# Optimization experiments

Measured on AMD Instinct MI355X. Metric: run time of the kernel, lower is better.

The kernel has to match this reference:

```python
import jax, jax.numpy as jnp
import numpy as np

B, SX, SL, D, H = 4, 4096, 256, 1024, 16
DH = D // H
LN_EPS = 1e-5
RMS_EPS = 1e-8


def layernorm(x, g, b):
    mu = jnp.mean(x, axis=-1, keepdims=True)
    var = jnp.mean(jnp.square(x - mu), axis=-1, keepdims=True)
    return (x - mu) * jax.lax.rsqrt(var + LN_EPS) * g + b


def rmsnorm(x, gamma):
    # torch: norm = ||x||_2 * dim^-0.5 ; x / clamp(norm, eps) * gamma
    norm = jnp.sqrt(jnp.sum(jnp.square(x), axis=-1, keepdims=True)) * (DH ** -0.5)
    return x / jnp.maximum(norm, RMS_EPS) * gamma


def setup_inputs() -> dict:
    key = jax.random.key(0)
    ks = jax.random.split(key, 6)
    s = 0.02
    return {
        "x": jax.random.normal(ks[0], (B, SX, D), jnp.float32),
        "latents": jax.random.normal(ks[1], (B, SL, D), jnp.float32),
        "mask_x": jnp.ones((B, SX), jnp.float32),
        "mask_latent": jnp.ones((B, SL), jnp.float32),
        "ln_x_g": jnp.ones((D,), jnp.float32),
        "ln_x_b": jnp.zeros((D,), jnp.float32),
        "ln_l_g": jnp.ones((D,), jnp.float32),
        "ln_l_b": jnp.zeros((D,), jnp.float32),
        "Wq": jax.random.normal(ks[2], (D, D), jnp.float32) * s,
        "Wkv": jax.random.normal(ks[3], (D, 2 * D), jnp.float32) * s,
        "qk_gamma": jnp.ones((DH,), jnp.float32),
        "Wo": jax.random.normal(ks[4], (D, D), jnp.float32) * s,
    }


def reference(x, latents, mask_x, mask_latent, ln_x_g, ln_x_b, ln_l_g, ln_l_b, Wq, Wkv, qk_gamma, Wo):
    xn = layernorm(x, ln_x_g, ln_x_b)                       # [B,SX,D]
    ln = layernorm(latents, ln_l_g, ln_l_b)                 # [B,SL,D]

    q = (ln @ Wq).reshape(B, SL, H, DH).transpose(0, 2, 1, 3)      # [B,H,SL,DH]
    kv_in = jnp.concatenate([xn, ln], axis=1)                      # [B,SX+SL,D]
    kv = kv_in @ Wkv
    Skv = SX + SL
    k = kv[..., :D].reshape(B, Skv, H, DH).transpose(0, 2, 1, 3)   # [B,H,Skv,DH]
    v = kv[..., D:].reshape(B, Skv, H, DH).transpose(0, 2, 1, 3)

    # NOTE: original code applies query_norm to BOTH q and k (faithful to source)
    q = rmsnorm(q, qk_gamma)
    k = rmsnorm(k, qk_gamma)

    scores = jnp.einsum("bhqd,bhkd->bhqk", q, k) / np.sqrt(DH)     # [B,H,SL,Skv]

    kv_mask = jnp.concatenate([mask_x, mask_latent], axis=1)       # [B,Skv]
    mask = kv_mask[:, None, :] * mask_latent[:, :, None]           # [B,SL,Skv]
    add_mask = (1.0 - mask)[:, None, :, :] * jnp.finfo(scores.dtype).min
    attn = jax.nn.softmax(scores + add_mask, axis=-1)

    y = jnp.einsum("bhqk,bhkd->bhqd", attn, v)                     # [B,H,SL,DH]
    y = y.transpose(0, 2, 1, 3).reshape(B, SL, D)
    return y @ Wo
```

## Files before the change

### kernel.cpp

```cpp
#include <hip/hip_runtime.h>

#define NB   4
#define SXX  4096
#define SLL  256
#define DD   1024
#define HH   16
#define DHH  64
#define SKV  4352
#define MKV  17408
#define NSPLIT 8

typedef __attribute__((ext_vector_type(8))) short bfrag;
typedef __attribute__((ext_vector_type(4))) float facc;

__device__ __forceinline__ unsigned short f2bf(float f){
  unsigned u = __builtin_bit_cast(unsigned, f);
  u = (u + 0x7fffu + ((u >> 16) & 1u)) >> 16;
  return (unsigned short)u;
}
__device__ __forceinline__ float bf2f(unsigned short h){
  unsigned u = ((unsigned)h) << 16;
  return __builtin_bit_cast(float, u);
}

#define GLOAD_LDS16(g, lds) __builtin_amdgcn_global_load_lds( \
    (const __attribute__((address_space(1))) unsigned int*)(const void*)(g), \
    (__attribute__((address_space(3))) unsigned int*)(void*)(lds), 16, 0, 0)

__global__ void wtrans3(const float* __restrict__ Wq, const float* __restrict__ Wkv,
                        const float* __restrict__ Wo, unsigned short* __restrict__ wqt,
                        unsigned short* __restrict__ wkvt, unsigned short* __restrict__ wot){
  __shared__ float t[32][33];
  int z = blockIdx.z;
  const float* in; unsigned short* out; int N;
  if (z == 0){ in = Wq;  out = wqt;  N = DD;   }
  else if (z == 1){ in = Wkv; out = wkvt; N = 2*DD; }
  else { in = Wo;  out = wot;  N = DD;   }
  int n0 = blockIdx.x * 32, k0 = blockIdx.y * 32;
  if (n0 >= N) return;
  int tx = threadIdx.x, ty = threadIdx.y;
  #pragma unroll
  for (int i = 0; i < 4; i++)
    t[ty + 8*i][tx] = in[(size_t)(k0 + ty + 8*i) * N + n0 + tx];
  __syncthreads();
  #pragma unroll
  for (int i = 0; i < 4; i++)
    out[(size_t)(n0 + ty + 8*i) * DD + k0 + tx] = f2bf(t[tx][ty + 8*i]);
}

__global__ void lnorm(const float* __restrict__ src, const float* __restrict__ g,
                      const float* __restrict__ bt, unsigned short* __restrict__ kvin,
                      unsigned short* __restrict__ dst2, int seq, int off){
  int row = blockIdx.x;
  int b = row / seq, s = row - b*seq;
  int t = threadIdx.x;
  const float4* rp = (const float4*)(src + (size_t)row * DD);
  float4 v = rp[t];
  float sum = v.x + v.y + v.z + v.w;
  float sq  = v.x*v.x + v.y*v.y + v.z*v.z + v.w*v.w;
  #pragma unroll
  for (int o = 32; o > 0; o >>= 1){ sum += __shfl_down(sum, o); sq += __shfl_down(sq, o); }
  __shared__ float ls[8];
  int w = t >> 6, l = t & 63;
  if (l == 0){ ls[w] = sum; ls[4 + w] = sq; }
  __syncthreads();
  sum = ls[0] + ls[1] + ls[2] + ls[3];
  sq  = ls[4] + ls[5] + ls[6] + ls[7];
  float mu  = sum * (1.f/DD);
  float var = sq * (1.f/DD) - mu*mu;
  float rs  = rsqrtf(var + 1e-5f);
  float4 gv = ((const float4*)g)[t];
  float4 bv = ((const float4*)bt)[t];
  ushort4 o4;
  o4.x = f2bf((v.x - mu)*rs*gv.x + bv.x);
  o4.y = f2bf((v.y - mu)*rs*gv.y + bv.y);
  o4.z = f2bf((v.z - mu)*rs*gv.z + bv.z);
  o4.w = f2bf((v.w - mu)*rs*gv.w + bv.w);
  *(ushort4*)(kvin + (size_t)(b*SKV + off + s) * DD + t*4) = o4;
  if (dst2) *(ushort4*)(dst2 + (size_t)row * DD + t*4) = o4;
}

__global__ __launch_bounds__(256) void gemm64(const unsigned short* __restrict__ A,
    const unsigned short* __restrict__ Bt, int M, int N, int K, float* __restrict__ outF){
  __shared__ unsigned short lA[64][72];
  __shared__ unsigned short lB[64][72];
  int n0 = blockIdx.x * 64, m0 = blockIdx.y * 64;
  int t = threadIdx.x, w = t >> 6, l = t & 63;
  int wr = (w >> 1) * 32, wc = (w & 1) * 32;
  int lr = l & 15, kq = (l >> 4) * 8;
  facc acc00 = (facc)0.f, acc01 = (facc)0.f, acc10 = (facc)0.f, acc11 = (facc)0.f;
  for (int k0 = 0; k0 < K; k0 += 64){
    #pragma unroll
    for (int cc = 0; cc < 2; cc++){
      int ch = t + cc*256;
      int row = ch >> 3, cg = (ch & 7) * 8;
      *(bfrag*)&lA[row][cg] = *(const bfrag*)&A[(size_t)(m0 + row) * K + k0 + cg];
      *(bfrag*)&lB[row][cg] = *(const bfrag*)&Bt[(size_t)(n0 + row) * K + k0 + cg];
    }
    __syncthreads();
    #pragma unroll
    for (int ks = 0; ks < 2; ks++){
      bfrag a0 = *(const bfrag*)&lA[wr + lr][ks*32 + kq];
      bfrag a1 = *(const bfrag*)&lA[wr + 16 + lr][ks*32 + kq];
      bfrag b0 = *(const bfrag*)&lB[wc + lr][ks*32 + kq];
      bfrag b1 = *(const bfrag*)&lB[wc + 16 + lr][ks*32 + kq];
      acc00 = __builtin_amdgcn_mfma_f32_16x16x32_bf16(a0, b0, acc00, 0, 0, 0);
      acc01 = __builtin_amdgcn_mfma_f32_16x16x32_bf16(a0, b1, acc01, 0, 0, 0);
      acc10 = __builtin_amdgcn_mfma_f32_16x16x32_bf16(a1, b0, acc10, 0, 0, 0);
      acc11 = __builtin_amdgcn_mfma_f32_16x16x32_bf16(a1, b1, acc11, 0, 0, 0);
    }
    __syncthreads();
  }
  int rl = (l >> 4) * 4, cl = l & 15;
  facc accs[2][2] = {{acc00, acc01},{acc10, acc11}};
  #pragma unroll
  for (int mt = 0; mt < 2; mt++)
  #pragma unroll
  for (int nt = 0; nt < 2; nt++)
  #pragma unroll
  for (int j = 0; j < 4; j++){
    int r = m0 + wr + mt*16 + rl + j;
    int c = n0 + wc + nt*16 + cl;
    outF[(size_t)r * N + c] = accs[mt][nt][j];
  }
}

__global__ __launch_bounds__(256) void gemm_q(const unsigned short* __restrict__ A,
    const unsigned short* __restrict__ Bt, const float* __restrict__ gamma,
    unsigned short* __restrict__ qn){
  __shared__ char smemb[18432];
  unsigned short* lA = (unsigned short*)smemb;
  unsigned short* lB = lA + 64*72;
  float* Cf = (float*)smemb;
  int h = blockIdx.x, n0 = h * 64, m0 = blockIdx.y * 64;
  int t = threadIdx.x, w = t >> 6, l = t & 63;
  int wr = (w >> 1) * 32, wc = (w & 1) * 32;
  int lr = l & 15, kq = (l >> 4) * 8;
  facc acc00 = (facc)0.f, acc01 = (facc)0.f, acc10 = (facc)0.f, acc11 = (facc)0.f;
  for (int k0 = 0; k0 < 1024; k0 += 64){
    #pragma unroll
    for (int cc = 0; cc < 2; cc++){
      int ch = t + cc*256;
      int row = ch >> 3, cg = (ch & 7) * 8;
      *(bfrag*)&lA[row*72 + cg] = *(const bfrag*)&A[(size_t)(m0 + row) * 1024 + k0 + cg];
      *(bfrag*)&lB[row*72 + cg] = *(const bfrag*)&Bt[(size_t)(n0 + row) * 1024 + k0 + cg];
    }
    __syncthreads();
    #pragma unroll
    for (int ks = 0; ks < 2; ks++){
      bfrag a0 = *(const bfrag*)&lA[(wr + lr)*72 + ks*32 + kq];
      bfrag a1 = *(const bfrag*)&lA[(wr + 16 + lr)*72 + ks*32 + kq];
      bfrag b0 = *(const bfrag*)&lB[(wc + lr)*72 + ks*32 + kq];
      bfrag b1 = *(const bfrag*)&lB[(wc + 16 + lr)*72 + ks*32 + kq];
      acc00 = __builtin_amdgcn_mfma_f32_16x16x32_bf16(a0, b0, acc00, 0, 0, 0);
      acc01 = __builtin_amdgcn_mfma_f32_16x16x32_bf16(a0, b1, acc01, 0, 0, 0);
      acc10 = __builtin_amdgcn_mfma_f32_16x16x32_bf16(a1, b0, acc10, 0, 0, 0);
      acc11 = __builtin_amdgcn_mfma_f32_16x16x32_bf16(a1, b1, acc11, 0, 0, 0);
    }
    __syncthreads();
  }
  int rl = (l >> 4) * 4, cl = l & 15;
  facc accs[2][2] = {{acc00, acc01},{acc10, acc11}};
  #pragma unroll
  for (int mt = 0; mt < 2; mt++)
  #pragma unroll
  for (int nt = 0; nt < 2; nt++)
  #pragma unroll
  for (int j = 0; j < 4; j++)
    Cf[(wr + mt*16 + rl + j)*66 + wc + nt*16 + cl] = accs[mt][nt][j];
  __syncthreads();
  if (t < 64){
    const float* src = &Cf[t*66];
    float ss = 0.f;
    #pragma unroll
    for (int d = 0; d < 64; d++){ float a = src[d]; ss = fmaf(a, a, ss); }
    float rv = 0.125f / fmaxf(sqrtf(ss) * 0.125f, 1e-8f);
    int r = m0 + t, b = r >> 8, sl = r & 255;
    unsigned short* dst = &qn[((size_t)(b*HH + h)*SLL + sl)*DHH];
    #pragma unroll
    for (int i = 0; i < 8; i++){
      ushort4 p; float g;
      g = gamma[i*8+0]; p.x = f2bf(src[i*8+0]*g*g*rv);
      g = gamma[i*8+1]; p.y = f2bf(src[i*8+1]*g*g*rv);
      g = gamma[i*8+2]; p.z = f2bf(src[i*8+2]*g*g*rv);
      g = gamma[i*8+3]; p.w = f2bf(src[i*8+3]*g*g*rv);
      ushort4 q;
      g = gamma[i*8+4]; q.x = f2bf(src[i*8+4]*g*g*rv);
      g = gamma[i*8+5]; q.y = f2bf(src[i*8+5]*g*g*rv);
      g = gamma[i*8+6]; q.z = f2bf(src[i*8+6]*g*g*rv);
      g = gamma[i*8+7]; q.w = f2bf(src[i*8+7]*g*g*rv);
      *(ushort4*)&dst[i*8]     = p;
      *(ushort4*)&dst[i*8 + 4] = q;
    }
  }
}

__global__ __launch_bounds__(256) void gemm_kv(const unsigned short* __restrict__ A,
    const unsigned short* __restrict__ Bt,
    const float* __restrict__ mask_x, const float* __restrict__ mask_lat,
    unsigned short* __restrict__ outK, unsigned short* __restrict__ outV,
    float* __restrict__ rkm){
  __shared__ unsigned short smem[128*136];
  unsigned short* lA = smem;
  unsigned short* lB = smem + 128*64;
  int n0 = blockIdx.x * 128, m0 = blockIdx.y * 128;
  int t = threadIdx.x, w = t >> 6, l = t & 63;
  int wr = (w >> 1) * 64, wc = (w & 1) * 64;
  int lr = l & 15, q2 = l >> 4;
  int r8 = l >> 3, u = l & 7;
  facc acc[4][4];
  #pragma unroll
  for (int mt = 0; mt < 4; mt++)
  #pragma unroll
  for (int nt = 0; nt < 4; nt++) acc[mt][nt] = (facc)0.f;
  const unsigned short* Ab = A  + (size_t)(m0 + w*32 + r8) * 1024 + (u ^ (r8 & 7)) * 8;
  const unsigned short* Bb = Bt + (size_t)(n0 + w*32 + r8) * 1024 + (u ^ (r8 & 7)) * 8;
  for (int k0 = 0; k0 < 1024; k0 += 64){
    #pragma unroll
    for (int i = 0; i < 4; i++){
      GLOAD_LDS16(Ab + (size_t)i*8*1024 + k0, &lA[(w*32 + i*8)*64]);
      GLOAD_LDS16(Bb + (size_t)i*8*1024 + k0, &lB[(w*32 + i*8)*64]);
    }
    __syncthreads();
    #pragma unroll
    for (int ks = 0; ks < 2; ks++){
      int su = ((ks*4 + q2) ^ (lr & 7)) * 8;
      bfrag av[4], bv[4];
      #pragma unroll
      for (int mt = 0; mt < 4; mt++) av[mt] = *(const bfrag*)&lA[(wr + mt*16 + lr)*64 + su];
      #pragma unroll
      for (int nt = 0; nt < 4; nt++) bv[nt] = *(const bfrag*)&lB[(wc + nt*16 + lr)*64 + su];
      #pragma unroll
      for (int mt = 0; mt < 4; mt++)
      #pragma unroll
      for (int nt = 0; nt < 4; nt++)
        acc[mt][nt] = __builtin_amdgcn_mfma_f32_16x16x32_bf16(av[mt], bv[nt], acc[mt][nt], 0, 0, 0);
    }
    __syncthreads();
  }
  int b = m0 / SKV, s0 = m0 - b*SKV;
  int rl = q2 * 4;
  if (blockIdx.x < 8){
    #pragma unroll
    for (int mt = 0; mt < 4; mt++)
    #pragma unroll
    for (int nt = 0; nt < 4; nt++)
    #pragma unroll
    for (int j = 0; j < 4; j++)
      smem[(wr + mt*16 + rl + j)*136 + wc + nt*16 + lr] = f2bf(acc[mt][nt][j]);
    __syncthreads();
    int s = t >> 1, hf = t & 1;
    int srow = s0 + s;
    float cm = (srow < SXX) ? mask_x[b*SXX + srow] : mask_lat[b*SLL + srow - SXX];
    const unsigned short* src = &smem[s*136 + hf*64];
    uint4 wv[8];
    #pragma unroll
    for (int i = 0; i < 8; i++) wv[i] = *(const uint4*)&src[i*8];
    float ss0 = 0.f, ss1 = 0.f;
    #pragma unroll
    for (int i = 0; i < 8; i++){
      const unsigned short* pp = (const unsigned short*)&wv[i];
      #pragma unroll
      for (int e = 0; e < 4; e++){
        float a = bf2f(pp[e]);     ss0 = fmaf(a, a, ss0);
        float c = bf2f(pp[e + 4]); ss1 = fmaf(c, c, ss1);
      }
    }
    float rv = 1.f / fmaxf(sqrtf(ss0 + ss1) * 0.125f, 1e-8f);
    int h = (n0 >> 6) + hf;
    unsigned short* dst = &outK[((size_t)(b*HH + h)*SKV + srow)*DHH];
    #pragma unroll
    for (int i = 0; i < 8; i++)
      *(uint4*)&dst[i*8] = wv[i];
    rkm[((size_t)(b*HH + h))*SKV + srow] = (cm != 0.f) ? rv : -1.f;
  } else {
    #pragma unroll
    for (int mt = 0; mt < 4; mt++)
    #pragma unroll
    for (int nt = 0; nt < 4; nt++){
      ushort4 p;
      p.x = f2bf(acc[mt][nt][0]); p.y = f2bf(acc[mt][nt][1]);
      p.z = f2bf(acc[mt][nt][2]); p.w = f2bf(acc[mt][nt][3]);
      *(ushort4*)&smem[(wc + nt*16 + lr)*136 + wr + mt*16 + rl] = p;
    }
    __syncthreads();
    int c = t >> 1, hf = t & 1;
    int hh = ((n0 - DD) >> 6) + (c >> 6), d = c & 63;
    const unsigned short* src = &smem[c*136 + hf*64];
    unsigned short* dst = &outV[((size_t)(b*HH + hh)*DHH + d)*SKV + s0 + hf*64];
    #pragma unroll
    for (int i = 0; i < 8; i++)
      *(uint4*)&dst[i*8] = *(const uint4*)&src[i*8];
  }
}

__global__ __launch_bounds__(256) void attn(const unsigned short* __restrict__ qn,
    const unsigned short* __restrict__ kbuf, const unsigned short* __restrict__ vT,
    const float* __restrict__ rkm, const float* __restrict__ mask_lat,
    float* __restrict__ Opart, float* __restrict__ lpart){
  int qt = blockIdx.x, bh = blockIdx.y, split = blockIdx.z;
  int b = bh >> 4;
  __shared__ unsigned short lP[4][2][16][68];
  int t = threadIdx.x, w = t >> 6, l = t & 63;
  int lr = l & 15, q2 = l >> 4, kq = q2 * 8;
  int q0 = qt * 128;
  bfrag aq0[2], aq1[2];
  float rm[2][4];
  #pragma unroll
  for (int tt = 0; tt < 2; tt++){
    const unsigned short* qbase = qn + ((size_t)bh * SLL + q0 + tt*64 + w*16 + lr) * DHH;
    aq0[tt] = *(const bfrag*)&qbase[kq];
    aq1[tt] = *(const bfrag*)&qbase[32 + kq];
    #pragma unroll
    for (int j = 0; j < 4; j++) rm[tt][j] = mask_lat[b*SLL + q0 + tt*64 + w*16 + q2*4 + j];
  }
  facc O[2][4];
  #pragma unroll
  for (int tt = 0; tt < 2; tt++)
  #pragma unroll
  for (int nt = 0; nt < 4; nt++) O[tt][nt] = (facc)0.f;
  float lsum[2][4];
  #pragma unroll
  for (int tt = 0; tt < 2; tt++)
  #pragma unroll
  for (int j = 0; j < 4; j++) lsum[tt][j] = 0.f;

  int t0 = (split * 68) / NSPLIT, t1 = ((split + 1) * 68) / NSPLIT;
  for (int kt = t0; kt < t1; kt++){
    int key0 = kt * 64;
    const unsigned short* kb = kbuf + ((size_t)bh * SKV + key0) * DHH;
    bfrag bk0[4], bk1[4]; float rk[4];
    #pragma unroll
    for (int nt = 0; nt < 4; nt++){
      bk0[nt] = *(const bfrag*)&kb[(nt*16 + lr)*DHH + kq];
      bk1[nt] = *(const bfrag*)&kb[(nt*16 + lr)*DHH + 32 + kq];
      rk[nt]  = rkm[(size_t)bh*SKV + key0 + nt*16 + lr];
    }
    facc S[2][4];
    #pragma unroll
    for (int tt = 0; tt < 2; tt++)
    #pragma unroll
    for (int nt = 0; nt < 4; nt++){
      S[tt][nt] = (facc)0.f;
      S[tt][nt] = __builtin_amdgcn_mfma_f32_16x16x32_bf16(aq0[tt], bk0[nt], S[tt][nt], 0, 0, 0);
      S[tt][nt] = __builtin_amdgcn_mfma_f32_16x16x32_bf16(aq1[tt], bk1[nt], S[tt][nt], 0, 0, 0);
    }
    const unsigned short* vb = vT + (size_t)bh * DHH * SKV + key0;
    bfrag bv0[4], bv1[4];
    #pragma unroll
    for (int nt = 0; nt < 4; nt++){
      bv0[nt] = *(const bfrag*)&vb[(size_t)(nt*16 + lr)*SKV + kq];
      bv1[nt] = *(const bfrag*)&vb[(size_t)(nt*16 + lr)*SKV + 32 + kq];
    }
    #pragma unroll
    for (int tt = 0; tt < 2; tt++){
      #pragma unroll
      for (int j = 0; j < 4; j++){
        float rs_ = 0.f;
        #pragma unroll
        for (int nt = 0; nt < 4; nt++){
          float x = S[tt][nt][j] * rk[nt];
          float sv = (rk[nt] >= 0.f && rm[tt][j] != 0.f) ? x : -3.0e38f;
          float p = __expf(sv - 8.0f);
          rs_ += p;
          lP[w][tt][q2*4 + j][nt*16 + lr] = f2bf(p);
        }
        lsum[tt][j] += rs_;
      }
    }
    __asm__ volatile("s_waitcnt lgkmcnt(0)" ::: "memory");
    bfrag ap0[2], ap1[2];
    #pragma unroll
    for (int tt = 0; tt < 2; tt++){
      ap0[tt] = *(const bfrag*)&lP[w][tt][lr][kq];
      ap1[tt] = *(const bfrag*)&lP[w][tt][lr][32 + kq];
    }
    #pragma unroll
    for (int nt = 0; nt < 4; nt++){
      #pragma unroll
      for (int tt = 0; tt < 2; tt++){
        O[tt][nt] = __builtin_amdgcn_mfma_f32_16x16x32_bf16(ap0[tt], bv0[nt], O[tt][nt], 0, 0, 0);
        O[tt][nt] = __builtin_amdgcn_mfma_f32_16x16x32_bf16(ap1[tt], bv1[nt], O[tt][nt], 0, 0, 0);
      }
    }
  }
  #pragma unroll
  for (int tt = 0; tt < 2; tt++)
  #pragma unroll
  for (int j = 0; j < 4; j++){
    float L = lsum[tt][j];
    L += __shfl_xor(L, 1); L += __shfl_xor(L, 2);
    L += __shfl_xor(L, 4); L += __shfl_xor(L, 8);
    int srow = q0 + tt*64 + w*16 + q2*4 + j;
    size_t obase = (((size_t)split*64 + bh)*SLL + srow)*DHH;
    #pragma unroll
    for (int nt = 0; nt < 4; nt++)
      Opart[obase + nt*16 + lr] = O[tt][nt][j];
    if (lr == 0)
      lpart[((size_t)split*64 + bh)*SLL + srow] = L;
  }
}

__global__ __launch_bounds__(256) void attn_combine(const float* __restrict__ Opart,
    const float* __restrict__ lpart, unsigned short* __restrict__ ybuf){
  int t = threadIdx.x, w = t >> 6, l = t & 63;
  int idx = blockIdx.x * 4 + w;
  int bh = idx >> 8, srow = idx & 255;
  int b = bh >> 4, h = bh & 15;
  float L = 0.f, acc = 0.f;
  #pragma unroll
  for (int s = 0; s < NSPLIT; s++){
    L   += lpart[((size_t)s*64 + bh)*SLL + srow];
    acc += Opart[(((size_t)s*64 + bh)*SLL + srow)*DHH + l];
  }
  ybuf[((size_t)b*SLL + srow)*DD + h*DHH + l] = f2bf(acc / L);
}

extern "C" void kernel_launch(void* const* d_in, const int* in_sizes, int n_in,
                              void* d_out, int out_size, void* d_ws, size_t ws_size,
                              hipStream_t stream) {
  const float* x        = (const float*)d_in[0];
  const float* latents  = (const float*)d_in[1];
  const float* mask_x   = (const float*)d_in[2];
  const float* mask_lat = (const float*)d_in[3];
  const float* ln_x_g   = (const float*)d_in[4];
  const float* ln_x_b   = (const float*)d_in[5];
  const float* ln_l_g   = (const float*)d_in[6];
  const float* ln_l_b   = (const float*)d_in[7];
  const float* Wq       = (const float*)d_in[8];
  const float* Wkv      = (const float*)d_in[9];
  const float* qk_gamma = (const float*)d_in[10];
  const float* Wo       = (const float*)d_in[11];
  float* out = (float*)d_out;

  char* wsb = (char*)d_ws;
  unsigned short* kvin  = (unsigned short*)(wsb + 0);
  unsigned short* lnlat = (unsigned short*)(wsb + 35651584);
  unsigned short* wqt   = (unsigned short*)(wsb + 37748736);
  unsigned short* wkvt  = (unsigned short*)(wsb + 39845888);
  unsigned short* wot   = (unsigned short*)(wsb + 44040192);
  unsigned short* qnb   = (unsigned short*)(wsb + 50331648);
  unsigned short* kbuf  = (unsigned short*)(wsb + 52428800);
  unsigned short* vT    = (unsigned short*)(wsb + 88080384);
  float*          rkm   = (float*)(wsb + 123731968);
  unsigned short* ybuf  = (unsigned short*)(wsb + 124846080);
  float*          Opart = (float*)(wsb + 0);
  float*          lpart = (float*)(wsb + 35651584);

  wtrans3<<<dim3(64, 32, 3), dim3(32, 8), 0, stream>>>(Wq, Wkv, Wo, wqt, wkvt, wot);

  lnorm<<<NB*SXX, 256, 0, stream>>>(x,       ln_x_g, ln_x_b, kvin, nullptr, SXX, 0);
  lnorm<<<NB*SLL, 256, 0, stream>>>(latents, ln_l_g, ln_l_b, kvin, lnlat,   SLL, SXX);

  gemm_q<<<dim3(16, 16), 256, 0, stream>>>(lnlat, wqt, qk_gamma, qnb);
  gemm_kv<<<dim3(16, 136), 256, 0, stream>>>(kvin, wkvt, mask_x, mask_lat, kbuf, vT, rkm);

  attn<<<dim3(SLL/128, NB*HH, NSPLIT), 256, 0, stream>>>(qnb, kbuf, vT, rkm, mask_lat, Opart, lpart);
  attn_combine<<<(NB*HH*SLL)/4, 256, 0, stream>>>(Opart, lpart, ybuf);

  gemm64<<<dim3(DD/64, (NB*SLL)/64), 256, 0, stream>>>(ybuf, wot, NB*SLL, DD, DD, out);
}
```

Baseline: 374.7 us.

## Pipeline KV GEMM with triple-buffered LDS, 256x128 tiles and XCD-aware block mapping

Rewrites the KV projection GEMM to use 512-thread workgroups that each compute a 256x128 tile. Global-to-LDS loads run two K-steps ahead through a triple-buffered LDS ring, with explicit vmcnt waits, sched barriers and raised priority around the MFMA bursts, so memory latency overlaps with compute. A 1D grid is remapped so neighbouring tiles land on the same XCD for better L2 reuse. The epilogues are adapted to the larger tile. The cost is much more LDS per block, which lowers occupancy, and tighter scheduling that depends on the compiler honouring the barriers.

```diff
diff --git a/kernel.cpp b/kernel.cpp
--- a/kernel.cpp
+++ b/kernel.cpp
@@ -195,64 +195,91 @@
   }
 }
 
-__global__ __launch_bounds__(256) void gemm_kv(const unsigned short* __restrict__ A,
+__global__ __launch_bounds__(512, 2) void gemm_kv(const unsigned short* __restrict__ A,
     const unsigned short* __restrict__ Bt,
     const float* __restrict__ mask_x, const float* __restrict__ mask_lat,
     unsigned short* __restrict__ outK, unsigned short* __restrict__ outV,
     float* __restrict__ rkm){
-  __shared__ unsigned short smem[128*136];
-  unsigned short* lA = smem;
-  unsigned short* lB = smem + 128*64;
-  int n0 = blockIdx.x * 128, m0 = blockIdx.y * 128;
+  __shared__ alignas(16) unsigned short lds[3 * 24576];
+  int bid = blockIdx.x;
+  int wg = (bid & 7) * 136 + (bid >> 3);
+  int m0 = (wg >> 4) * 256, n0 = (wg & 15) * 128;
   int t = threadIdx.x, w = t >> 6, l = t & 63;
-  int wr = (w >> 1) * 64, wc = (w & 1) * 64;
+  int wm = w >> 1, wn = w & 1;
   int lr = l & 15, q2 = l >> 4;
   int r8 = l >> 3, u = l & 7;
+  int swz = (u ^ (r8 & 7)) * 8;
+  const unsigned short* Ag = A  + (size_t)(m0 + w*8 + r8) * 1024 + swz;
+  const unsigned short* Bg = Bt + (size_t)(n0 + w*8 + r8) * 1024 + swz;
+
   facc acc[4][4];
   #pragma unroll
   for (int mt = 0; mt < 4; mt++)
   #pragma unroll
   for (int nt = 0; nt < 4; nt++) acc[mt][nt] = (facc)0.f;
-  const unsigned short* Ab = A  + (size_t)(m0 + w*32 + r8) * 1024 + (u ^ (r8 & 7)) * 8;
-  const unsigned short* Bb = Bt + (size_t)(n0 + w*32 + r8) * 1024 + (u ^ (r8 & 7)) * 8;
-  for (int k0 = 0; k0 < 1024; k0 += 64){
-    #pragma unroll
-    for (int i = 0; i < 4; i++){
-      GLOAD_LDS16(Ab + (size_t)i*8*1024 + k0, &lA[(w*32 + i*8)*64]);
-      GLOAD_LDS16(Bb + (size_t)i*8*1024 + k0, &lB[(w*32 + i*8)*64]);
-    }
-    __syncthreads();
-    #pragma unroll
-    for (int ks = 0; ks < 2; ks++){
-      int su = ((ks*4 + q2) ^ (lr & 7)) * 8;
-      bfrag av[4], bv[4];
-      #pragma unroll
-      for (int mt = 0; mt < 4; mt++) av[mt] = *(const bfrag*)&lA[(wr + mt*16 + lr)*64 + su];
-      #pragma unroll
-      for (int nt = 0; nt < 4; nt++) bv[nt] = *(const bfrag*)&lB[(wc + nt*16 + lr)*64 + su];
-      #pragma unroll
-      for (int mt = 0; mt < 4; mt++)
-      #pragma unroll
-      for (int nt = 0; nt < 4; nt++)
-        acc[mt][nt] = __builtin_amdgcn_mfma_f32_16x16x32_bf16(av[mt], bv[nt], acc[mt][nt], 0, 0, 0);
-    }
-    __syncthreads();
-  }
+
+#define SBAR __builtin_amdgcn_sched_barrier(0)
+#define KV_BARRIER do { SBAR; __builtin_amdgcn_s_barrier(); SBAR; } while(0)
+#define KV_STA(j, i) GLOAD_LDS16(Ag + (size_t)(i)*65536 + (j)*64, \
+    &lds[((j) % 3)*24576 + (i)*4096 + w*512])
+#define KV_STB(j, i) GLOAD_LDS16(Bg + (size_t)(i)*65536 + (j)*64, \
+    &lds[((j) % 3)*24576 + 16384 + (i)*4096 + w*512])
+#define KV_LDFRAG(j, ks) { \
+    const unsigned short* pA = &lds[((j) % 3)*24576 + (wm*64 + lr)*64 + (((ks)*4 + q2) ^ (lr & 7))*8]; \
+    const unsigned short* pB = &lds[((j) % 3)*24576 + 16384 + (wn*64 + lr)*64 + (((ks)*4 + q2) ^ (lr & 7))*8]; \
+    av[0] = *(const bfrag*)(pA);        av[1] = *(const bfrag*)(pA + 1024); \
+    av[2] = *(const bfrag*)(pA + 2048); av[3] = *(const bfrag*)(pA + 3072); \
+    bv[0] = *(const bfrag*)(pB);        bv[1] = *(const bfrag*)(pB + 1024); \
+    bv[2] = *(const bfrag*)(pB + 2048); bv[3] = *(const bfrag*)(pB + 3072); }
+#define KV_MFMA do { \
+    __builtin_amdgcn_s_setprio(1); \
+    _Pragma("unroll") \
+    for (int mt = 0; mt < 4; mt++){ \
+      _Pragma("unroll") \
+      for (int nt = 0; nt < 4; nt++) \
+        acc[mt][nt] = __builtin_amdgcn_mfma_f32_16x16x32_bf16(av[mt], bv[nt], acc[mt][nt], 0, 0, 0); } \
+    __builtin_amdgcn_s_setprio(0); } while(0)
+
+  KV_STA(0,0); KV_STA(0,1); KV_STA(0,2); KV_STA(0,3); KV_STB(0,0); KV_STB(0,1);
+  KV_STA(1,0); KV_STA(1,1); KV_STA(1,2); KV_STA(1,3); KV_STB(1,0); KV_STB(1,1);
+  __asm__ volatile("s_waitcnt vmcnt(6)" ::: "memory");
+  KV_BARRIER;
+
+  bfrag av[4], bv[4];
+  #pragma unroll
+  for (int j = 0; j < 16; j++){
+    KV_LDFRAG(j, 0);
+    if (j < 14){ KV_STA(j+2, 0); KV_STA(j+2, 1); KV_STB(j+2, 0); }
+    KV_BARRIER;
+    KV_MFMA;
+    KV_BARRIER;
+    KV_LDFRAG(j, 1);
+    if (j < 14){ KV_STA(j+2, 2); KV_STA(j+2, 3); KV_STB(j+2, 1); }
+    KV_BARRIER;
+    KV_MFMA;
+    if (j < 14)       { __asm__ volatile("s_waitcnt vmcnt(6)" ::: "memory"); }
+    else if (j == 14) { __asm__ volatile("s_waitcnt vmcnt(0)" ::: "memory"); }
+    KV_BARRIER;
+  }
+#undef KV_STA
+#undef KV_STB
+#undef KV_LDFRAG
+#undef KV_MFMA
+
   int b = m0 / SKV, s0 = m0 - b*SKV;
-  int rl = q2 * 4;
-  if (blockIdx.x < 8){
+  if (n0 < DD){
     #pragma unroll
     for (int mt = 0; mt < 4; mt++)
     #pragma unroll
     for (int nt = 0; nt < 4; nt++)
     #pragma unroll
     for (int j = 0; j < 4; j++)
-      smem[(wr + mt*16 + rl + j)*136 + wc + nt*16 + lr] = f2bf(acc[mt][nt][j]);
+      lds[(wm*64 + mt*16 + q2*4 + j)*136 + wn*64 + nt*16 + lr] = f2bf(acc[mt][nt][j]);
     __syncthreads();
     int s = t >> 1, hf = t & 1;
     int srow = s0 + s;
     float cm = (srow < SXX) ? mask_x[b*SXX + srow] : mask_lat[b*SLL + srow - SXX];
-    const unsigned short* src = &smem[s*136 + hf*64];
+    const unsigned short* src = &lds[s*136 + hf*64];
     uint4 wv[8];
     #pragma unroll
     for (int i = 0; i < 8; i++) wv[i] = *(const uint4*)&src[i*8];
@@ -281,13 +308,13 @@
       ushort4 p;
       p.x = f2bf(acc[mt][nt][0]); p.y = f2bf(acc[mt][nt][1]);
       p.z = f2bf(acc[mt][nt][2]); p.w = f2bf(acc[mt][nt][3]);
-      *(ushort4*)&smem[(wc + nt*16 + lr)*136 + wr + mt*16 + rl] = p;
-    }
-    __syncthreads();
-    int c = t >> 1, hf = t & 1;
+      *(ushort4*)&lds[(wn*64 + nt*16 + lr)*264 + wm*64 + mt*16 + q2*4] = p;
+    }
+    __syncthreads();
+    int c = t >> 2, sq = t & 3;
     int hh = ((n0 - DD) >> 6) + (c >> 6), d = c & 63;
-    const unsigned short* src = &smem[c*136 + hf*64];
-    unsigned short* dst = &outV[((size_t)(b*HH + hh)*DHH + d)*SKV + s0 + hf*64];
+    const unsigned short* src = &lds[c*264 + sq*64];
+    unsigned short* dst = &outV[((size_t)(b*HH + hh)*DHH + d)*SKV + s0 + sq*64];
     #pragma unroll
     for (int i = 0; i < 8; i++)
       *(uint4*)&dst[i*8] = *(const uint4*)&src[i*8];
@@ -453,7 +480,7 @@
   lnorm<<<NB*SLL, 256, 0, stream>>>(latents, ln_l_g, ln_l_b, kvin, lnlat,   SLL, SXX);
 
   gemm_q<<<dim3(16, 16), 256, 0, stream>>>(lnlat, wqt, qk_gamma, qnb);
-  gemm_kv<<<dim3(16, 136), 256, 0, stream>>>(kvin, wkvt, mask_x, mask_lat, kbuf, vT, rkm);
+  gemm_kv<<<dim3(1088), 512, 0, stream>>>(kvin, wkvt, mask_x, mask_lat, kbuf, vT, rkm);
 
   attn<<<dim3(SLL/128, NB*HH, NSPLIT), 256, 0, stream>>>(qnb, kbuf, vT, rkm, mask_lat, Opart, lpart);
   attn_combine<<<(NB*HH*SLL)/4, 256, 0, stream>>>(Opart, lpart, ybuf);
```

Result: no change. 369.1 us (-1.5%).
